# Kernel optimization log

Hardware: AMD Instinct MI355X
Metric: run time of the kernel (lower is better)

## Reference

```python
import jax, jax.numpy as jnp
import numpy as np

NUM_TABLES = 10
EMB_DIM = 3
VOCAB = 1_000_000
N_IDX = 4_000_000
N_BAGS = 100_000


def setup_inputs() -> dict:
    key = jax.random.key(0)
    k_idx, k_off, k_w = jax.random.split(key, 3)
    eb_input = jax.random.randint(k_idx, (N_IDX,), 0, VOCAB, dtype=jnp.int64)
    # EmbeddingBag offsets: sorted, first element must be 0, values in [0, N_IDX)
    eb_offset = jnp.sort(jax.random.randint(k_off, (N_BAGS,), 0, N_IDX, dtype=jnp.int64))
    eb_offset = eb_offset.at[0].set(0)
    # torch.nn.EmbeddingBag default init: N(0, 1)
    W = jax.random.normal(k_w, (NUM_TABLES, VOCAB, EMB_DIM), dtype=jnp.float32)
    return {"eb_input": eb_input, "eb_offset": eb_offset, "W": W}


def _bag_sums(eb_input, eb_offset, W):
    # segment id for each index position: bag b covers [offset[b], offset[b+1])
    n = eb_input.shape[0]
    seg = jnp.searchsorted(eb_offset, jnp.arange(n), side="right") - 1  # [N]
    gathered = W[:, eb_input, :]  # [T, N, D] irregular gather
    # sum-pool per bag for every table
    per_bag = jax.vmap(lambda g: jax.ops.segment_sum(g, seg, num_segments=eb_offset.shape[0]))(gathered)  # [T, B, D]
    return per_bag


def reference(eb_input, eb_offset, W):
    per_bag = _bag_sums(eb_input, eb_offset, W)  # [10, B, 3]
    outs = [per_bag[i] for i in range(NUM_TABLES)]
    outs[5] = jnp.sum(outs[5], axis=1, keepdims=True)  # [B, 1]
    outs[6] = jnp.sum(outs[6], axis=1, keepdims=True)  # [B, 1]
    cat = jnp.concatenate(outs, axis=1)  # [B, 26]
    return jnp.sum(cat, axis=0)  # [26]
```

## Files before the change

kernel.cpp:

```cpp
#include <hip/hip_runtime.h>

#define VOCAB 1000000
#define NUM_TABLES 10
#define OUT_SIZE 26
#define BUCKET_BITS 12
#define BPB 4096
#define NBUCKETS 245
#define CHUNK 4096
#define MAXSRC 1024
#define NGROUPS (VOCAB / 4)
#define RBLK ((NGROUPS + 255) / 256)
#define PSTRIDE 1024


__global__ void __launch_bounds__(256) scatter_kernel(
    const int* __restrict__ idx, int n,
    unsigned short* __restrict__ scat,
    unsigned int* __restrict__ gs32)
{
    __shared__ unsigned int lcount[256];
    __shared__ unsigned int sc[256];
    __shared__ unsigned short stage[CHUNK];
    const int tid = threadIdx.x;
    lcount[tid] = 0u;
    __syncthreads();

    const int4* idx4 = (const int4*)idx;
    const int n4 = n >> 2;
    const int base4 = blockIdx.x * (CHUNK / 4);
    int4 q[4];
    bool val[4];
    unsigned rank[16];
    unsigned bkt[16];
#pragma unroll
    for (int j = 0; j < 4; ++j) {
        int i4 = base4 + j * 256 + tid;
        val[j] = (i4 < n4);
        if (val[j]) q[j] = idx4[i4];
    }
#pragma unroll
    for (int j = 0; j < 4; ++j) {
        if (val[j]) {
            unsigned v[4] = {(unsigned)q[j].x, (unsigned)q[j].y, (unsigned)q[j].z, (unsigned)q[j].w};
#pragma unroll
            for (int e = 0; e < 4; ++e) {
                bkt[j * 4 + e] = v[e] >> BUCKET_BITS;
                rank[j * 4 + e] = atomicAdd(&lcount[bkt[j * 4 + e]], 1u);
            }
        }
    }
    unsigned trank[3], tbkt[3];
    int tcnt = 0;
    if (blockIdx.x == gridDim.x - 1 && tid == 0) {
        for (int i = n4 * 4; i < n; ++i) {
            unsigned u = (unsigned)idx[i];
            tbkt[tcnt] = u >> BUCKET_BITS;
            trank[tcnt] = atomicAdd(&lcount[tbkt[tcnt]], 1u);
            ++tcnt;
        }
    }
    __syncthreads();
    unsigned cnt = (tid < NBUCKETS) ? lcount[tid] : 0u;
    sc[tid] = cnt;
    __syncthreads();
#pragma unroll
    for (int off = 1; off < 256; off <<= 1) {
        unsigned v = sc[tid];
        unsigned a = (tid >= off) ? sc[tid - off] : 0u;
        __syncthreads();
        sc[tid] = v + a;
        __syncthreads();
    }
    unsigned excl = sc[tid] - cnt;
    if (tid < NBUCKETS) gs32[tid * MAXSRC + blockIdx.x] = excl | (cnt << 16);
    lcount[tid] = excl;
    __syncthreads();
#pragma unroll
    for (int j = 0; j < 4; ++j) {
        if (val[j]) {
            unsigned v[4] = {(unsigned)q[j].x, (unsigned)q[j].y, (unsigned)q[j].z, (unsigned)q[j].w};
#pragma unroll
            for (int e = 0; e < 4; ++e) {
                unsigned k = j * 4 + e;
                stage[lcount[bkt[k]] + rank[k]] = (unsigned short)(v[e] & (BPB - 1));
            }
        }
    }
    if (blockIdx.x == gridDim.x - 1 && tid == 0) {
        for (int i = 0; i < tcnt; ++i) {
            unsigned u = (unsigned)idx[n4 * 4 + i];
            stage[lcount[tbkt[i]] + trank[i]] = (unsigned short)(u & (BPB - 1));
        }
    }
    __syncthreads();
    uint4* dst = (uint4*)(scat + (size_t)blockIdx.x * CHUNK);
    const uint4* src = (const uint4*)stage;
#pragma unroll
    for (int j = 0; j < 2; ++j) dst[j * 256 + tid] = src[j * 256 + tid];
}

__global__ void __launch_bounds__(512) bucket_hist_kernel(
    const unsigned short* __restrict__ scat,
    const unsigned int* __restrict__ gs32, int nsrc,
    unsigned short* __restrict__ h0,
    unsigned short* __restrict__ h1)
{
    __shared__ unsigned int h[BPB];
    const int b = blockIdx.x >> 1;
    const int qh = blockIdx.x & 1;
    const int tid = threadIdx.x;
    const int half = (nsrc + 1) >> 1;
    for (int i = tid; i < BPB; i += 512) h[i] = 0u;
    __syncthreads();
    const int s0 = qh * half;
    const int scount = min(half, nsrc - s0);
    for (int t = tid; t < scount; t += 512) {
        const int src = s0 + t;
        unsigned g32 = gs32[b * MAXSRC + src];
        unsigned s = g32 & 0xffffu, c = g32 >> 16;
        const unsigned short* p = scat + (size_t)src * CHUNK + s;
        unsigned k = 0;
        for (; k + 4 <= c; k += 4) {
            unsigned short a0 = p[k], a1 = p[k + 1], a2 = p[k + 2], a3 = p[k + 3];
            atomicAdd(&h[a0], 1u);
            atomicAdd(&h[a1], 1u);
            atomicAdd(&h[a2], 1u);
            atomicAdd(&h[a3], 1u);
        }
        for (; k < c; ++k) atomicAdd(&h[p[k]], 1u);
    }
    __syncthreads();
    unsigned short* dst = (qh ? h1 : h0) + (size_t)b * BPB;
    const int base = tid * 8;
    uint4 o;
    o.x = h[base + 0] | (h[base + 1] << 16);
    o.y = h[base + 2] | (h[base + 3] << 16);
    o.z = h[base + 4] | (h[base + 5] << 16);
    o.w = h[base + 6] | (h[base + 7] << 16);
    ((uint4*)dst)[tid] = o;
}

__device__ inline float wave_reduce(float v) {
#pragma unroll
    for (int o = 32; o > 0; o >>= 1) v += __shfl_down(v, o, 64);
    return v;
}

__global__ void __launch_bounds__(256) reduce_kernel(
    const float* __restrict__ W,
    const unsigned short* __restrict__ h0,
    const unsigned short* __restrict__ h1,
    float* __restrict__ partials)
{
    const int g = blockIdx.x * 256 + (int)threadIdx.x;
    float acc[NUM_TABLES][3];
#pragma unroll
    for (int t = 0; t < NUM_TABLES; ++t) { acc[t][0] = 0.f; acc[t][1] = 0.f; acc[t][2] = 0.f; }
    if (g < NGROUPS) {
        uint2 pa = ((const uint2*)h0)[g];
        uint2 pb = ((const uint2*)h1)[g];
        float c0 = (float)((pa.x & 0xffffu) + (pb.x & 0xffffu));
        float c1 = (float)((pa.x >> 16) + (pb.x >> 16));
        float c2 = (float)((pa.y & 0xffffu) + (pb.y & 0xffffu));
        float c3 = (float)((pa.y >> 16) + (pb.y >> 16));
        const size_t w4base = 3 * (size_t)g;
#pragma unroll
        for (int t = 0; t < NUM_TABLES; ++t) {
            const float4* W4 = ((const float4*)W) + (size_t)t * 750000 + w4base;
            float4 w0 = W4[0];
            float4 w1 = W4[1];
            float4 w2 = W4[2];
            acc[t][0] = c0 * w0.x + c1 * w0.w + c2 * w1.z + c3 * w2.y;
            acc[t][1] = c0 * w0.y + c1 * w1.x + c2 * w1.w + c3 * w2.z;
            acc[t][2] = c0 * w0.z + c1 * w1.y + c2 * w2.x + c3 * w2.w;
        }
    }
    __shared__ float sf[30 * 4];
    const int wave = threadIdx.x >> 6, lane = threadIdx.x & 63;
#pragma unroll
    for (int t = 0; t < NUM_TABLES; ++t)
#pragma unroll
        for (int d = 0; d < 3; ++d) {
            float v = wave_reduce(acc[t][d]);
            if (lane == 0) sf[(t * 3 + d) * 4 + wave] = v;
        }
    __syncthreads();
    if (threadIdx.x < 30) {
        const float* p = &sf[threadIdx.x * 4];
        partials[threadIdx.x * PSTRIDE + blockIdx.x] = p[0] + p[1] + p[2] + p[3];
    }
}

__global__ void __launch_bounds__(1024) final_kernel(const float* __restrict__ partials,
                                                     int nblk, float* __restrict__ out) {
    __shared__ float ts[32];
    const int tid = threadIdx.x;
    const int srs = tid >> 5;
    const int j = tid & 31;
    float v = 0.f;
    if (srs < 30) {
        const float* p = partials + (size_t)srs * PSTRIDE;
        for (int k = j; k < nblk; k += 32) v += p[k];
    }
#pragma unroll
    for (int off = 16; off > 0; off >>= 1) v += __shfl_down(v, off, 32);
    if (j == 0 && srs < 30) ts[srs] = v;
    __syncthreads();
    if (tid < OUT_SIZE) {
        float r;
        if (tid < 15) r = ts[tid];
        else if (tid == 15) r = ts[15] + ts[16] + ts[17];
        else if (tid == 16) r = ts[18] + ts[19] + ts[20];
        else r = ts[tid + 4];
        out[tid] = r;
    }
}


__global__ void zero_kernel_fb(unsigned int* __restrict__ hist, float* __restrict__ out) {
    int i = blockIdx.x * blockDim.x + threadIdx.x;
    int n4 = VOCAB / 4;
    if (i < n4) ((uint4*)hist)[i] = make_uint4(0u, 0u, 0u, 0u);
    if (i < OUT_SIZE) out[i] = 0.0f;
}

__global__ void hist_kernel_fb(const int* __restrict__ idx, unsigned int* __restrict__ hist, int n) {
    int i = blockIdx.x * blockDim.x + threadIdx.x;
    int i4 = i * 4;
    if (i4 + 3 < n) {
        int4 v = ((const int4*)idx)[i];
        atomicAdd(&hist[v.x], 1u);
        atomicAdd(&hist[v.y], 1u);
        atomicAdd(&hist[v.z], 1u);
        atomicAdd(&hist[v.w], 1u);
    } else {
        for (int j = i4; j < n; ++j) atomicAdd(&hist[idx[j]], 1u);
    }
}

__global__ void __launch_bounds__(256) reduce_kernel_fb(const float* __restrict__ W,
                                                        const unsigned int* __restrict__ hist,
                                                        float* __restrict__ out) {
    const int t = blockIdx.x / 64;
    const int b = blockIdx.x % 64;
    const float4* __restrict__ W4 = (const float4*)(W + (size_t)t * VOCAB * 3);
    const uint4* __restrict__ h4 = (const uint4*)hist;
    float a0 = 0.f, a1 = 0.f, a2 = 0.f;
    const int stride = 64 * 256;
    for (int g = b * 256 + (int)threadIdx.x; g < NGROUPS; g += stride) {
        uint4 c4 = h4[g];
        float4 w0 = W4[3 * g + 0];
        float4 w1 = W4[3 * g + 1];
        float4 w2 = W4[3 * g + 2];
        float c0 = (float)c4.x, c1 = (float)c4.y, c2 = (float)c4.z, c3 = (float)c4.w;
        a0 += c0 * w0.x + c1 * w0.w + c2 * w1.z + c3 * w2.y;
        a1 += c0 * w0.y + c1 * w1.x + c2 * w1.w + c3 * w2.z;
        a2 += c0 * w0.z + c1 * w1.y + c2 * w2.x + c3 * w2.w;
    }
    a0 = wave_reduce(a0);
    a1 = wave_reduce(a1);
    a2 = wave_reduce(a2);
    __shared__ float s[3][4];
    int wave = threadIdx.x >> 6;
    int lane = threadIdx.x & 63;
    if (lane == 0) { s[0][wave] = a0; s[1][wave] = a1; s[2][wave] = a2; }
    __syncthreads();
    if (threadIdx.x == 0) {
        float r0 = s[0][0] + s[0][1] + s[0][2] + s[0][3];
        float r1 = s[1][0] + s[1][1] + s[1][2] + s[1][3];
        float r2 = s[2][0] + s[2][1] + s[2][2] + s[2][3];
        if (t == 5) atomicAdd(&out[15], r0 + r1 + r2);
        else if (t == 6) atomicAdd(&out[16], r0 + r1 + r2);
        else {
            int base = (t < 5) ? t * 3 : 17 + (t - 7) * 3;
            atomicAdd(&out[base + 0], r0);
            atomicAdd(&out[base + 1], r1);
            atomicAdd(&out[base + 2], r2);
        }
    }
}


extern "C" void kernel_launch(void* const* d_in, const int* in_sizes, int n_in,
                              void* d_out, int out_size, void* d_ws, size_t ws_size,
                              hipStream_t stream) {
    const int* eb_input = (const int*)d_in[0];
    const float* W = (const float*)d_in[2];
    float* out = (float*)d_out;
    int n_idx = in_sizes[0];

    const int nsrc = (n_idx + CHUNK - 1) / CHUNK;
    const size_t scat_bytes = (size_t)MAXSRC * CHUNK * 2;
    const size_t gs_off = scat_bytes;
    const size_t gs_bytes = (size_t)NBUCKETS * MAXSRC * 4;
    const size_t h0_off = gs_off + gs_bytes;
    const size_t hpart_bytes = (size_t)NBUCKETS * BPB * 2;
    const size_t h1_off = h0_off + hpart_bytes;
    const size_t part_off = (h1_off + hpart_bytes + 255) & ~(size_t)255;
    const size_t need = part_off + (size_t)30 * PSTRIDE * 4;

    if (nsrc <= MAXSRC && ws_size >= need) {
        unsigned short* scat = (unsigned short*)d_ws;
        unsigned int* gs32 = (unsigned int*)((char*)d_ws + gs_off);
        unsigned short* h0 = (unsigned short*)((char*)d_ws + h0_off);
        unsigned short* h1 = (unsigned short*)((char*)d_ws + h1_off);
        float* partials = (float*)((char*)d_ws + part_off);

        scatter_kernel<<<nsrc, 256, 0, stream>>>(eb_input, n_idx, scat, gs32);
        bucket_hist_kernel<<<NBUCKETS * 2, 512, 0, stream>>>(scat, gs32, nsrc, h0, h1);
        reduce_kernel<<<RBLK, 256, 0, stream>>>(W, h0, h1, partials);
        final_kernel<<<1, 1024, 0, stream>>>(partials, RBLK, out);
    } else {
        unsigned int* hist = (unsigned int*)d_ws;
        int zblocks = (VOCAB / 4 + 255) / 256;
        zero_kernel_fb<<<zblocks, 256, 0, stream>>>(hist, out);
        int hthreads = (n_idx + 3) / 4;
        int hblocks = (hthreads + 255) / 256;
        hist_kernel_fb<<<hblocks, 256, 0, stream>>>(eb_input, hist, n_idx);
        reduce_kernel_fb<<<NUM_TABLES * 64, 256, 0, stream>>>(W, hist, out);
    }
}
```

Baseline: 221.6 us.

## Split reduce kernel across table halves with grid-stride loop over vocab groups

The reduce kernel now launches 1024 blocks, split into two halves that each handle 5 of the 10 tables. Within a half, each thread walks the vocab groups with a grid-stride loop. This halves the per-thread accumulator count, which lowers register pressure and should raise occupancy. The cost is that each half re-reads the histogram counts, and the final kernel still sums 30 partial rows but now with 512 entries each.

```diff
diff --git a/kernel.cpp b/kernel.cpp
--- a/kernel.cpp
+++ b/kernel.cpp
@@ -9,7 +9,7 @@
 #define CHUNK 4096
 #define MAXSRC 1024
 #define NGROUPS (VOCAB / 4)
-#define RBLK ((NGROUPS + 255) / 256)
+#define RBLK_HALF 512
 #define PSTRIDE 1024
 
 
@@ -152,11 +152,14 @@
     const unsigned short* __restrict__ h1,
     float* __restrict__ partials)
 {
-    const int g = blockIdx.x * 256 + (int)threadIdx.x;
-    float acc[NUM_TABLES][3];
-#pragma unroll
-    for (int t = 0; t < NUM_TABLES; ++t) { acc[t][0] = 0.f; acc[t][1] = 0.f; acc[t][2] = 0.f; }
-    if (g < NGROUPS) {
+    const int half = blockIdx.x >> 9;
+    const int b = blockIdx.x & (RBLK_HALF - 1);
+    const int tbase = half * 5;
+    float acc[5][3];
+#pragma unroll
+    for (int t = 0; t < 5; ++t) { acc[t][0] = 0.f; acc[t][1] = 0.f; acc[t][2] = 0.f; }
+    const int stride = RBLK_HALF * 256;
+    for (int g = b * 256 + (int)threadIdx.x; g < NGROUPS; g += stride) {
         uint2 pa = ((const uint2*)h0)[g];
         uint2 pb = ((const uint2*)h1)[g];
         float c0 = (float)((pa.x & 0xffffu) + (pb.x & 0xffffu));
@@ -165,29 +168,29 @@
         float c3 = (float)((pa.y >> 16) + (pb.y >> 16));
         const size_t w4base = 3 * (size_t)g;
 #pragma unroll
-        for (int t = 0; t < NUM_TABLES; ++t) {
-            const float4* W4 = ((const float4*)W) + (size_t)t * 750000 + w4base;
+        for (int t = 0; t < 5; ++t) {
+            const float4* W4 = ((const float4*)W) + (size_t)(tbase + t) * 750000 + w4base;
             float4 w0 = W4[0];
             float4 w1 = W4[1];
             float4 w2 = W4[2];
-            acc[t][0] = c0 * w0.x + c1 * w0.w + c2 * w1.z + c3 * w2.y;
-            acc[t][1] = c0 * w0.y + c1 * w1.x + c2 * w1.w + c3 * w2.z;
-            acc[t][2] = c0 * w0.z + c1 * w1.y + c2 * w2.x + c3 * w2.w;
-        }
-    }
-    __shared__ float sf[30 * 4];
+            acc[t][0] += c0 * w0.x + c1 * w0.w + c2 * w1.z + c3 * w2.y;
+            acc[t][1] += c0 * w0.y + c1 * w1.x + c2 * w1.w + c3 * w2.z;
+            acc[t][2] += c0 * w0.z + c1 * w1.y + c2 * w2.x + c3 * w2.w;
+        }
+    }
+    __shared__ float sf[15 * 4];
     const int wave = threadIdx.x >> 6, lane = threadIdx.x & 63;
 #pragma unroll
-    for (int t = 0; t < NUM_TABLES; ++t)
+    for (int t = 0; t < 5; ++t)
 #pragma unroll
         for (int d = 0; d < 3; ++d) {
             float v = wave_reduce(acc[t][d]);
             if (lane == 0) sf[(t * 3 + d) * 4 + wave] = v;
         }
     __syncthreads();
-    if (threadIdx.x < 30) {
+    if (threadIdx.x < 15) {
         const float* p = &sf[threadIdx.x * 4];
-        partials[threadIdx.x * PSTRIDE + blockIdx.x] = p[0] + p[1] + p[2] + p[3];
+        partials[(half * 15 + threadIdx.x) * PSTRIDE + b] = p[0] + p[1] + p[2] + p[3];
     }
 }
 
@@ -308,8 +311,8 @@
 
         scatter_kernel<<<nsrc, 256, 0, stream>>>(eb_input, n_idx, scat, gs32);
         bucket_hist_kernel<<<NBUCKETS * 2, 512, 0, stream>>>(scat, gs32, nsrc, h0, h1);
-        reduce_kernel<<<RBLK, 256, 0, stream>>>(W, h0, h1, partials);
-        final_kernel<<<1, 1024, 0, stream>>>(partials, RBLK, out);
+        reduce_kernel<<<2 * RBLK_HALF, 256, 0, stream>>>(W, h0, h1, partials);
+        final_kernel<<<1, 1024, 0, stream>>>(partials, RBLK_HALF, out);
     } else {
         unsigned int* hist = (unsigned int*)d_ws;
         int zblocks = (VOCAB / 4 + 255) / 256;
```

After: 216.8 us. 2.2% less time.

## Fuse four histogram-reduce kernels into one cooperative persistent kernel

Applied to the files above, without the earlier changes.

Replaces the scatter, bucket-histogram, weighted-reduce and final-sum kernels with a single cooperative kernel of 512 blocks that loops over work items and separates phases with grid.sync(). The goal is to remove three kernel launch gaps and tail effects between stages. In exchange it fixes occupancy at 512x256 threads: the histogram phase now uses 256 threads instead of 512 per bucket, and the reduce phase uses a strided per-table layout. Grid-wide barriers add their own latency.

```diff
diff --git a/kernel.cpp b/kernel.cpp
--- a/kernel.cpp
+++ b/kernel.cpp
@@ -1,4 +1,7 @@
 #include <hip/hip_runtime.h>
+#include <hip/hip_cooperative_groups.h>
+
+namespace cg = cooperative_groups;
 
 #define VOCAB 1000000
 #define NUM_TABLES 10
@@ -9,136 +12,8 @@
 #define CHUNK 4096
 #define MAXSRC 1024
 #define NGROUPS (VOCAB / 4)
-#define RBLK ((NGROUPS + 255) / 256)
-#define PSTRIDE 1024
-
-
-__global__ void __launch_bounds__(256) scatter_kernel(
-    const int* __restrict__ idx, int n,
-    unsigned short* __restrict__ scat,
-    unsigned int* __restrict__ gs32)
-{
-    __shared__ unsigned int lcount[256];
-    __shared__ unsigned int sc[256];
-    __shared__ unsigned short stage[CHUNK];
-    const int tid = threadIdx.x;
-    lcount[tid] = 0u;
-    __syncthreads();
-
-    const int4* idx4 = (const int4*)idx;
-    const int n4 = n >> 2;
-    const int base4 = blockIdx.x * (CHUNK / 4);
-    int4 q[4];
-    bool val[4];
-    unsigned rank[16];
-    unsigned bkt[16];
-#pragma unroll
-    for (int j = 0; j < 4; ++j) {
-        int i4 = base4 + j * 256 + tid;
-        val[j] = (i4 < n4);
-        if (val[j]) q[j] = idx4[i4];
-    }
-#pragma unroll
-    for (int j = 0; j < 4; ++j) {
-        if (val[j]) {
-            unsigned v[4] = {(unsigned)q[j].x, (unsigned)q[j].y, (unsigned)q[j].z, (unsigned)q[j].w};
-#pragma unroll
-            for (int e = 0; e < 4; ++e) {
-                bkt[j * 4 + e] = v[e] >> BUCKET_BITS;
-                rank[j * 4 + e] = atomicAdd(&lcount[bkt[j * 4 + e]], 1u);
-            }
-        }
-    }
-    unsigned trank[3], tbkt[3];
-    int tcnt = 0;
-    if (blockIdx.x == gridDim.x - 1 && tid == 0) {
-        for (int i = n4 * 4; i < n; ++i) {
-            unsigned u = (unsigned)idx[i];
-            tbkt[tcnt] = u >> BUCKET_BITS;
-            trank[tcnt] = atomicAdd(&lcount[tbkt[tcnt]], 1u);
-            ++tcnt;
-        }
-    }
-    __syncthreads();
-    unsigned cnt = (tid < NBUCKETS) ? lcount[tid] : 0u;
-    sc[tid] = cnt;
-    __syncthreads();
-#pragma unroll
-    for (int off = 1; off < 256; off <<= 1) {
-        unsigned v = sc[tid];
-        unsigned a = (tid >= off) ? sc[tid - off] : 0u;
-        __syncthreads();
-        sc[tid] = v + a;
-        __syncthreads();
-    }
-    unsigned excl = sc[tid] - cnt;
-    if (tid < NBUCKETS) gs32[tid * MAXSRC + blockIdx.x] = excl | (cnt << 16);
-    lcount[tid] = excl;
-    __syncthreads();
-#pragma unroll
-    for (int j = 0; j < 4; ++j) {
-        if (val[j]) {
-            unsigned v[4] = {(unsigned)q[j].x, (unsigned)q[j].y, (unsigned)q[j].z, (unsigned)q[j].w};
-#pragma unroll
-            for (int e = 0; e < 4; ++e) {
-                unsigned k = j * 4 + e;
-                stage[lcount[bkt[k]] + rank[k]] = (unsigned short)(v[e] & (BPB - 1));
-            }
-        }
-    }
-    if (blockIdx.x == gridDim.x - 1 && tid == 0) {
-        for (int i = 0; i < tcnt; ++i) {
-            unsigned u = (unsigned)idx[n4 * 4 + i];
-            stage[lcount[tbkt[i]] + trank[i]] = (unsigned short)(u & (BPB - 1));
-        }
-    }
-    __syncthreads();
-    uint4* dst = (uint4*)(scat + (size_t)blockIdx.x * CHUNK);
-    const uint4* src = (const uint4*)stage;
-#pragma unroll
-    for (int j = 0; j < 2; ++j) dst[j * 256 + tid] = src[j * 256 + tid];
-}
-
-__global__ void __launch_bounds__(512) bucket_hist_kernel(
-    const unsigned short* __restrict__ scat,
-    const unsigned int* __restrict__ gs32, int nsrc,
-    unsigned short* __restrict__ h0,
-    unsigned short* __restrict__ h1)
-{
-    __shared__ unsigned int h[BPB];
-    const int b = blockIdx.x >> 1;
-    const int qh = blockIdx.x & 1;
-    const int tid = threadIdx.x;
-    const int half = (nsrc + 1) >> 1;
-    for (int i = tid; i < BPB; i += 512) h[i] = 0u;
-    __syncthreads();
-    const int s0 = qh * half;
-    const int scount = min(half, nsrc - s0);
-    for (int t = tid; t < scount; t += 512) {
-        const int src = s0 + t;
-        unsigned g32 = gs32[b * MAXSRC + src];
-        unsigned s = g32 & 0xffffu, c = g32 >> 16;
-        const unsigned short* p = scat + (size_t)src * CHUNK + s;
-        unsigned k = 0;
-        for (; k + 4 <= c; k += 4) {
-            unsigned short a0 = p[k], a1 = p[k + 1], a2 = p[k + 2], a3 = p[k + 3];
-            atomicAdd(&h[a0], 1u);
-            atomicAdd(&h[a1], 1u);
-            atomicAdd(&h[a2], 1u);
-            atomicAdd(&h[a3], 1u);
-        }
-        for (; k < c; ++k) atomicAdd(&h[p[k]], 1u);
-    }
-    __syncthreads();
-    unsigned short* dst = (qh ? h1 : h0) + (size_t)b * BPB;
-    const int base = tid * 8;
-    uint4 o;
-    o.x = h[base + 0] | (h[base + 1] << 16);
-    o.y = h[base + 2] | (h[base + 3] << 16);
-    o.z = h[base + 4] | (h[base + 5] << 16);
-    o.w = h[base + 6] | (h[base + 7] << 16);
-    ((uint4*)dst)[tid] = o;
-}
+#define GBLOCKS 512
+#define GTHREADS 256
 
 __device__ inline float wave_reduce(float v) {
 #pragma unroll
@@ -146,73 +21,206 @@
     return v;
 }
 
-__global__ void __launch_bounds__(256) reduce_kernel(
+
+__global__ void __launch_bounds__(GTHREADS) mega_kernel(
+    const int* __restrict__ idx, int n, int nchunks,
     const float* __restrict__ W,
-    const unsigned short* __restrict__ h0,
-    const unsigned short* __restrict__ h1,
-    float* __restrict__ partials)
+    unsigned short* __restrict__ scat,
+    unsigned int* __restrict__ gs32,
+    unsigned short* __restrict__ h0,
+    unsigned short* __restrict__ h1,
+    float* __restrict__ partials,
+    float* __restrict__ out)
 {
-    const int g = blockIdx.x * 256 + (int)threadIdx.x;
-    float acc[NUM_TABLES][3];
-#pragma unroll
-    for (int t = 0; t < NUM_TABLES; ++t) { acc[t][0] = 0.f; acc[t][1] = 0.f; acc[t][2] = 0.f; }
-    if (g < NGROUPS) {
-        uint2 pa = ((const uint2*)h0)[g];
-        uint2 pb = ((const uint2*)h1)[g];
-        float c0 = (float)((pa.x & 0xffffu) + (pb.x & 0xffffu));
-        float c1 = (float)((pa.x >> 16) + (pb.x >> 16));
-        float c2 = (float)((pa.y & 0xffffu) + (pb.y & 0xffffu));
-        float c3 = (float)((pa.y >> 16) + (pb.y >> 16));
-        const size_t w4base = 3 * (size_t)g;
-#pragma unroll
-        for (int t = 0; t < NUM_TABLES; ++t) {
-            const float4* W4 = ((const float4*)W) + (size_t)t * 750000 + w4base;
-            float4 w0 = W4[0];
-            float4 w1 = W4[1];
-            float4 w2 = W4[2];
-            acc[t][0] = c0 * w0.x + c1 * w0.w + c2 * w1.z + c3 * w2.y;
-            acc[t][1] = c0 * w0.y + c1 * w1.x + c2 * w1.w + c3 * w2.z;
-            acc[t][2] = c0 * w0.z + c1 * w1.y + c2 * w2.x + c3 * w2.w;
-        }
-    }
-    __shared__ float sf[30 * 4];
-    const int wave = threadIdx.x >> 6, lane = threadIdx.x & 63;
-#pragma unroll
-    for (int t = 0; t < NUM_TABLES; ++t)
-#pragma unroll
-        for (int d = 0; d < 3; ++d) {
-            float v = wave_reduce(acc[t][d]);
-            if (lane == 0) sf[(t * 3 + d) * 4 + wave] = v;
-        }
-    __syncthreads();
-    if (threadIdx.x < 30) {
-        const float* p = &sf[threadIdx.x * 4];
-        partials[threadIdx.x * PSTRIDE + blockIdx.x] = p[0] + p[1] + p[2] + p[3];
-    }
-}
-
-__global__ void __launch_bounds__(1024) final_kernel(const float* __restrict__ partials,
-                                                     int nblk, float* __restrict__ out) {
-    __shared__ float ts[32];
+    __shared__ unsigned int smem[4096];
+    cg::grid_group grid = cg::this_grid();
     const int tid = threadIdx.x;
-    const int srs = tid >> 5;
-    const int j = tid & 31;
-    float v = 0.f;
-    if (srs < 30) {
-        const float* p = partials + (size_t)srs * PSTRIDE;
-        for (int k = j; k < nblk; k += 32) v += p[k];
-    }
-#pragma unroll
-    for (int off = 16; off > 0; off >>= 1) v += __shfl_down(v, off, 32);
-    if (j == 0 && srs < 30) ts[srs] = v;
-    __syncthreads();
-    if (tid < OUT_SIZE) {
-        float r;
-        if (tid < 15) r = ts[tid];
-        else if (tid == 15) r = ts[15] + ts[16] + ts[17];
-        else if (tid == 16) r = ts[18] + ts[19] + ts[20];
-        else r = ts[tid + 4];
-        out[tid] = r;
+
+    {
+        unsigned int* lcount = smem;
+        unsigned int* sc = smem + 256;
+        unsigned short* stage = (unsigned short*)(smem + 512);
+        const int4* idx4 = (const int4*)idx;
+        const int n4 = n >> 2;
+        for (int c = blockIdx.x; c < nchunks; c += GBLOCKS) {
+            lcount[tid] = 0u;
+            __syncthreads();
+            const int base4 = c * (CHUNK / 4);
+            int4 q[4];
+            bool val[4];
+            unsigned rank[16], bkt[16];
+#pragma unroll
+            for (int j = 0; j < 4; ++j) {
+                int i4 = base4 + j * 256 + tid;
+                val[j] = (i4 < n4);
+                if (val[j]) q[j] = idx4[i4];
+            }
+#pragma unroll
+            for (int j = 0; j < 4; ++j) {
+                if (val[j]) {
+                    unsigned v[4] = {(unsigned)q[j].x, (unsigned)q[j].y,
+                                     (unsigned)q[j].z, (unsigned)q[j].w};
+#pragma unroll
+                    for (int e = 0; e < 4; ++e) {
+                        bkt[j * 4 + e] = v[e] >> BUCKET_BITS;
+                        rank[j * 4 + e] = atomicAdd(&lcount[bkt[j * 4 + e]], 1u);
+                    }
+                }
+            }
+            unsigned trank[3], tbkt[3];
+            int tcnt = 0;
+            if (c == nchunks - 1 && tid == 0) {
+                for (int i = n4 * 4; i < n; ++i) {
+                    unsigned u = (unsigned)idx[i];
+                    tbkt[tcnt] = u >> BUCKET_BITS;
+                    trank[tcnt] = atomicAdd(&lcount[tbkt[tcnt]], 1u);
+                    ++tcnt;
+                }
+            }
+            __syncthreads();
+            unsigned cnt = (tid < NBUCKETS) ? lcount[tid] : 0u;
+            sc[tid] = cnt;
+            __syncthreads();
+#pragma unroll
+            for (int off = 1; off < 256; off <<= 1) {
+                unsigned v = sc[tid];
+                unsigned a = (tid >= off) ? sc[tid - off] : 0u;
+                __syncthreads();
+                sc[tid] = v + a;
+                __syncthreads();
+            }
+            unsigned excl = sc[tid] - cnt;
+            if (tid < NBUCKETS) gs32[tid * MAXSRC + c] = excl | (cnt << 16);
+            lcount[tid] = excl;
+            __syncthreads();
+#pragma unroll
+            for (int j = 0; j < 4; ++j) {
+                if (val[j]) {
+                    unsigned v[4] = {(unsigned)q[j].x, (unsigned)q[j].y,
+                                     (unsigned)q[j].z, (unsigned)q[j].w};
+#pragma unroll
+                    for (int e = 0; e < 4; ++e) {
+                        unsigned k = j * 4 + e;
+                        stage[lcount[bkt[k]] + rank[k]] = (unsigned short)(v[e] & (BPB - 1));
+                    }
+                }
+            }
+            if (c == nchunks - 1 && tid == 0) {
+                for (int i = 0; i < tcnt; ++i) {
+                    unsigned u = (unsigned)idx[n4 * 4 + i];
+                    stage[lcount[tbkt[i]] + trank[i]] = (unsigned short)(u & (BPB - 1));
+                }
+            }
+            __syncthreads();
+            uint4* dst = (uint4*)(scat + (size_t)c * CHUNK);
+            const uint4* src = (const uint4*)stage;
+            dst[tid] = src[tid];
+            dst[256 + tid] = src[256 + tid];
+            __syncthreads();
+        }
+    }
+    grid.sync();
+
+    {
+        unsigned int* h = smem;
+        const int half = (nchunks + 1) >> 1;
+        for (int j = blockIdx.x; j < 2 * NBUCKETS; j += GBLOCKS) {
+            const int b = j >> 1, qh = j & 1;
+            for (int i = tid; i < BPB; i += GTHREADS) h[i] = 0u;
+            __syncthreads();
+            const int s0 = qh * half;
+            const int scount = min(half, nchunks - s0);
+            for (int t = tid; t < scount; t += GTHREADS) {
+                const int srcc = s0 + t;
+                unsigned g32 = gs32[b * MAXSRC + srcc];
+                unsigned s = g32 & 0xffffu, cc = g32 >> 16;
+                const unsigned short* p = scat + (size_t)srcc * CHUNK + s;
+                unsigned k = 0;
+                for (; k + 4 <= cc; k += 4) {
+                    unsigned short a0 = p[k], a1 = p[k + 1], a2 = p[k + 2], a3 = p[k + 3];
+                    atomicAdd(&h[a0], 1u);
+                    atomicAdd(&h[a1], 1u);
+                    atomicAdd(&h[a2], 1u);
+                    atomicAdd(&h[a3], 1u);
+                }
+                for (; k < cc; ++k) atomicAdd(&h[p[k]], 1u);
+            }
+            __syncthreads();
+            unsigned short* dsth = (qh ? h1 : h0) + (size_t)b * BPB;
+#pragma unroll
+            for (int r = 0; r < 2; ++r) {
+                int base = (r * 256 + tid) * 8;
+                uint4 o;
+                o.x = h[base + 0] | (h[base + 1] << 16);
+                o.y = h[base + 2] | (h[base + 3] << 16);
+                o.z = h[base + 4] | (h[base + 5] << 16);
+                o.w = h[base + 6] | (h[base + 7] << 16);
+                ((uint4*)dsth)[r * 256 + tid] = o;
+            }
+            __syncthreads();
+        }
+    }
+    grid.sync();
+
+    {
+        float* sf = (float*)smem;
+        const int wave = tid >> 6, lane = tid & 63;
+        for (int job = blockIdx.x; job < NUM_TABLES * 256; job += GBLOCKS) {
+            const int t = job >> 8, slice = job & 255;
+            const float4* W4 = ((const float4*)W) + (size_t)t * 750000;
+            float a0 = 0.f, a1 = 0.f, a2 = 0.f;
+            for (int g = slice * 256 + tid; g < NGROUPS; g += 65536) {
+                uint2 pa = ((const uint2*)h0)[g];
+                uint2 pb = ((const uint2*)h1)[g];
+                float c0 = (float)((pa.x & 0xffffu) + (pb.x & 0xffffu));
+                float c1 = (float)((pa.x >> 16) + (pb.x >> 16));
+                float c2 = (float)((pa.y & 0xffffu) + (pb.y & 0xffffu));
+                float c3 = (float)((pa.y >> 16) + (pb.y >> 16));
+                float4 w0 = W4[3 * (size_t)g + 0];
+                float4 w1 = W4[3 * (size_t)g + 1];
+                float4 w2 = W4[3 * (size_t)g + 2];
+                a0 += c0 * w0.x + c1 * w0.w + c2 * w1.z + c3 * w2.y;
+                a1 += c0 * w0.y + c1 * w1.x + c2 * w1.w + c3 * w2.z;
+                a2 += c0 * w0.z + c1 * w1.y + c2 * w2.x + c3 * w2.w;
+            }
+            a0 = wave_reduce(a0);
+            a1 = wave_reduce(a1);
+            a2 = wave_reduce(a2);
+            if (lane == 0) { sf[wave] = a0; sf[4 + wave] = a1; sf[8 + wave] = a2; }
+            __syncthreads();
+            if (tid < 3) {
+                const float* p = sf + tid * 4;
+                partials[(t * 3 + tid) * 256 + slice] = p[0] + p[1] + p[2] + p[3];
+            }
+            __syncthreads();
+        }
+    }
+    grid.sync();
+
+    if (blockIdx.x == 0) {
+        float* red = (float*)smem;
+        float* ts = (float*)smem + 256;
+        float v = 0.f;
+        if (tid < 240) {
+            const int srs = tid >> 3, jj = tid & 7;
+            const float* p = partials + srs * 256;
+            for (int k = jj; k < 256; k += 8) v += p[k];
+        }
+        red[tid] = v;
+        __syncthreads();
+        if (tid < 30) {
+            const float* p = red + tid * 8;
+            ts[tid] = p[0] + p[1] + p[2] + p[3] + p[4] + p[5] + p[6] + p[7];
+        }
+        __syncthreads();
+        if (tid < OUT_SIZE) {
+            float r;
+            if (tid < 15) r = ts[tid];
+            else if (tid == 15) r = ts[15] + ts[16] + ts[17];
+            else if (tid == 16) r = ts[18] + ts[19] + ts[20];
+            else r = ts[tid + 4];
+            out[tid] = r;
+        }
     }
 }
 
@@ -289,7 +297,7 @@
     float* out = (float*)d_out;
     int n_idx = in_sizes[0];
 
-    const int nsrc = (n_idx + CHUNK - 1) / CHUNK;
+    const int nchunks = (n_idx + CHUNK - 1) / CHUNK;
     const size_t scat_bytes = (size_t)MAXSRC * CHUNK * 2;
     const size_t gs_off = scat_bytes;
     const size_t gs_bytes = (size_t)NBUCKETS * MAXSRC * 4;
@@ -297,19 +305,22 @@
     const size_t hpart_bytes = (size_t)NBUCKETS * BPB * 2;
     const size_t h1_off = h0_off + hpart_bytes;
     const size_t part_off = (h1_off + hpart_bytes + 255) & ~(size_t)255;
-    const size_t need = part_off + (size_t)30 * PSTRIDE * 4;
-
-    if (nsrc <= MAXSRC && ws_size >= need) {
+    const size_t need = part_off + (size_t)30 * 256 * 4;
+
+    if (nchunks <= MAXSRC && ws_size >= need) {
         unsigned short* scat = (unsigned short*)d_ws;
         unsigned int* gs32 = (unsigned int*)((char*)d_ws + gs_off);
         unsigned short* h0 = (unsigned short*)((char*)d_ws + h0_off);
         unsigned short* h1 = (unsigned short*)((char*)d_ws + h1_off);
         float* partials = (float*)((char*)d_ws + part_off);
 
-        scatter_kernel<<<nsrc, 256, 0, stream>>>(eb_input, n_idx, scat, gs32);
-        bucket_hist_kernel<<<NBUCKETS * 2, 512, 0, stream>>>(scat, gs32, nsrc, h0, h1);
-        reduce_kernel<<<RBLK, 256, 0, stream>>>(W, h0, h1, partials);
-        final_kernel<<<1, 1024, 0, stream>>>(partials, RBLK, out);
+        const int* idxp = eb_input;
+        int n = n_idx, nch = nchunks;
+        const float* Wp = W;
+        float* outp = out;
+        void* args[] = {&idxp, &n, &nch, &Wp, &scat, &gs32, &h0, &h1, &partials, &outp};
+        hipLaunchCooperativeKernel(mega_kernel, dim3(GBLOCKS), dim3(GTHREADS),
+                                   args, 0, stream);
     } else {
         unsigned int* hist = (unsigned int*)d_ws;
         int zblocks = (VOCAB / 4 + 255) / 256;
```

New measurement: 396.1 us. +78.7%, slower.

## Split reduce kernel per table with multi-group tiles; read histogram pairs as 32-bit

Applied to the files above, without the earlier changes.

The reduce kernel now gives each block one table and a tile of 1024 vertex groups, four per thread, instead of every thread covering all ten tables. This cuts register pressure and the 30 wave reductions per block down to three, and raises the number of blocks. The trade-off is that the histogram counts are reloaded once per table. The bucket histogram loop also reads the 16-bit bucket entries as 32-bit pairs, with alignment fixups at both ends, to halve the number of load instructions.

```diff
diff --git a/kernel.cpp b/kernel.cpp
--- a/kernel.cpp
+++ b/kernel.cpp
@@ -9,8 +9,8 @@
 #define CHUNK 4096
 #define MAXSRC 1024
 #define NGROUPS (VOCAB / 4)
-#define RBLK ((NGROUPS + 255) / 256)
-#define PSTRIDE 1024
+#define RTILES 245
+#define PSTRIDE 256
 
 
 __global__ void __launch_bounds__(256) scatter_kernel(
@@ -119,15 +119,22 @@
         unsigned g32 = gs32[b * MAXSRC + src];
         unsigned s = g32 & 0xffffu, c = g32 >> 16;
         const unsigned short* p = scat + (size_t)src * CHUNK + s;
+        if ((s & 1u) && c) { atomicAdd(&h[p[0]], 1u); ++p; --c; }
+        const unsigned* p32 = (const unsigned*)p;
+        unsigned n2 = c >> 1;
         unsigned k = 0;
-        for (; k + 4 <= c; k += 4) {
-            unsigned short a0 = p[k], a1 = p[k + 1], a2 = p[k + 2], a3 = p[k + 3];
-            atomicAdd(&h[a0], 1u);
-            atomicAdd(&h[a1], 1u);
-            atomicAdd(&h[a2], 1u);
-            atomicAdd(&h[a3], 1u);
-        }
-        for (; k < c; ++k) atomicAdd(&h[p[k]], 1u);
+        for (; k + 4 <= n2; k += 4) {
+            unsigned u0 = p32[k], u1 = p32[k + 1], u2 = p32[k + 2], u3 = p32[k + 3];
+            atomicAdd(&h[u0 & 0xffffu], 1u); atomicAdd(&h[u0 >> 16], 1u);
+            atomicAdd(&h[u1 & 0xffffu], 1u); atomicAdd(&h[u1 >> 16], 1u);
+            atomicAdd(&h[u2 & 0xffffu], 1u); atomicAdd(&h[u2 >> 16], 1u);
+            atomicAdd(&h[u3 & 0xffffu], 1u); atomicAdd(&h[u3 >> 16], 1u);
+        }
+        for (; k < n2; ++k) {
+            unsigned u = p32[k];
+            atomicAdd(&h[u & 0xffffu], 1u); atomicAdd(&h[u >> 16], 1u);
+        }
+        if (c & 1u) atomicAdd(&h[p[c - 1]], 1u);
     }
     __syncthreads();
     unsigned short* dst = (qh ? h1 : h0) + (size_t)b * BPB;
@@ -152,42 +159,52 @@
     const unsigned short* __restrict__ h1,
     float* __restrict__ partials)
 {
-    const int g = blockIdx.x * 256 + (int)threadIdx.x;
-    float acc[NUM_TABLES][3];
-#pragma unroll
-    for (int t = 0; t < NUM_TABLES; ++t) { acc[t][0] = 0.f; acc[t][1] = 0.f; acc[t][2] = 0.f; }
-    if (g < NGROUPS) {
-        uint2 pa = ((const uint2*)h0)[g];
-        uint2 pb = ((const uint2*)h1)[g];
-        float c0 = (float)((pa.x & 0xffffu) + (pb.x & 0xffffu));
-        float c1 = (float)((pa.x >> 16) + (pb.x >> 16));
-        float c2 = (float)((pa.y & 0xffffu) + (pb.y & 0xffffu));
-        float c3 = (float)((pa.y >> 16) + (pb.y >> 16));
-        const size_t w4base = 3 * (size_t)g;
-#pragma unroll
-        for (int t = 0; t < NUM_TABLES; ++t) {
-            const float4* W4 = ((const float4*)W) + (size_t)t * 750000 + w4base;
-            float4 w0 = W4[0];
-            float4 w1 = W4[1];
-            float4 w2 = W4[2];
-            acc[t][0] = c0 * w0.x + c1 * w0.w + c2 * w1.z + c3 * w2.y;
-            acc[t][1] = c0 * w0.y + c1 * w1.x + c2 * w1.w + c3 * w2.z;
-            acc[t][2] = c0 * w0.z + c1 * w1.y + c2 * w2.x + c3 * w2.w;
-        }
-    }
-    __shared__ float sf[30 * 4];
-    const int wave = threadIdx.x >> 6, lane = threadIdx.x & 63;
-#pragma unroll
-    for (int t = 0; t < NUM_TABLES; ++t)
-#pragma unroll
-        for (int d = 0; d < 3; ++d) {
-            float v = wave_reduce(acc[t][d]);
-            if (lane == 0) sf[(t * 3 + d) * 4 + wave] = v;
-        }
-    __syncthreads();
-    if (threadIdx.x < 30) {
-        const float* p = &sf[threadIdx.x * 4];
-        partials[threadIdx.x * PSTRIDE + blockIdx.x] = p[0] + p[1] + p[2] + p[3];
+    const int t = blockIdx.x / RTILES;
+    const int tile = blockIdx.x % RTILES;
+    const int g0 = tile * 1024 + (int)threadIdx.x;
+    const float4* __restrict__ W4 = ((const float4*)W) + (size_t)t * 750000;
+    const uint2* __restrict__ H0 = (const uint2*)h0;
+    const uint2* __restrict__ H1 = (const uint2*)h1;
+    float a0 = 0.f, a1 = 0.f, a2 = 0.f;
+    float b0 = 0.f, b1 = 0.f, b2 = 0.f;
+#pragma unroll
+    for (int i = 0; i < 4; ++i) {
+        int g = g0 + i * 256;
+        bool valid = (g < NGROUPS);
+        int gc = valid ? g : (NGROUPS - 1);
+        uint2 pa = H0[gc];
+        uint2 pb = H1[gc];
+        float4 w0 = W4[3 * (size_t)gc + 0];
+        float4 w1 = W4[3 * (size_t)gc + 1];
+        float4 w2 = W4[3 * (size_t)gc + 2];
+        float m = valid ? 1.0f : 0.0f;
+        unsigned sx = pa.x + pb.x;
+        unsigned sy = pa.y + pb.y;
+        float c0 = m * (float)(sx & 0xffffu), c1 = m * (float)(sx >> 16);
+        float c2 = m * (float)(sy & 0xffffu), c3 = m * (float)(sy >> 16);
+        if (i & 1) {
+            b0 += c0 * w0.x + c1 * w0.w + c2 * w1.z + c3 * w2.y;
+            b1 += c0 * w0.y + c1 * w1.x + c2 * w1.w + c3 * w2.z;
+            b2 += c0 * w0.z + c1 * w1.y + c2 * w2.x + c3 * w2.w;
+        } else {
+            a0 += c0 * w0.x + c1 * w0.w + c2 * w1.z + c3 * w2.y;
+            a1 += c0 * w0.y + c1 * w1.x + c2 * w1.w + c3 * w2.z;
+            a2 += c0 * w0.z + c1 * w1.y + c2 * w2.x + c3 * w2.w;
+        }
+    }
+    a0 += b0; a1 += b1; a2 += b2;
+    a0 = wave_reduce(a0);
+    a1 = wave_reduce(a1);
+    a2 = wave_reduce(a2);
+    __shared__ float s[3][4];
+    int wave = threadIdx.x >> 6;
+    int lane = threadIdx.x & 63;
+    if (lane == 0) { s[0][wave] = a0; s[1][wave] = a1; s[2][wave] = a2; }
+    __syncthreads();
+    if (threadIdx.x == 0) {
+        partials[(t * 3 + 0) * PSTRIDE + tile] = s[0][0] + s[0][1] + s[0][2] + s[0][3];
+        partials[(t * 3 + 1) * PSTRIDE + tile] = s[1][0] + s[1][1] + s[1][2] + s[1][3];
+        partials[(t * 3 + 2) * PSTRIDE + tile] = s[2][0] + s[2][1] + s[2][2] + s[2][3];
     }
 }
 
@@ -308,8 +325,8 @@
 
         scatter_kernel<<<nsrc, 256, 0, stream>>>(eb_input, n_idx, scat, gs32);
         bucket_hist_kernel<<<NBUCKETS * 2, 512, 0, stream>>>(scat, gs32, nsrc, h0, h1);
-        reduce_kernel<<<RBLK, 256, 0, stream>>>(W, h0, h1, partials);
-        final_kernel<<<1, 1024, 0, stream>>>(partials, RBLK, out);
+        reduce_kernel<<<NUM_TABLES * RTILES, 256, 0, stream>>>(W, h0, h1, partials);
+        final_kernel<<<1, 1024, 0, stream>>>(partials, RTILES, out);
     } else {
         unsigned int* hist = (unsigned int*)d_ws;
         int zblocks = (VOCAB / 4 + 255) / 256;
```

Result: faster. 210.4 us (-5.1%).
